# Kernel optimization log

Measured on AMD Instinct MI355X. Metric: run time of the kernel, lower is better.

The kernel has to match this reference:

```python
import jax, jax.numpy as jnp
import numpy as np

EPSILON = 0.001  # clip margin from HParams.epsilon
_EPS32 = float(np.finfo(np.float32).eps)  # added to bound in create_ops


@jax.custom_jvp
def floor_ste(x):
    """Floor with Straight-Through-Estimator gradient."""
    return jnp.floor(x)


@floor_ste.defjvp
def _floor_ste_jvp(primals, tangents):
    (x,), (t,) = primals, tangents
    return jnp.floor(x), t


def _binarize(x, bound):
    # (-inf,0) -> -bound/2, [0,inf) -> +bound/2, via scale-clip-floor-STE
    scale = 1.0 / bound
    clip_bound = 1.0 - EPSILON
    y = jnp.clip(x * scale, -clip_bound, clip_bound)
    y = floor_ste(y) + 0.5
    return (y / scale).astype(x.dtype)


def setup_inputs() -> dict:
    key = jax.random.key(0)
    k1, k2 = jax.random.split(key, 2)
    B, S, D, F = 4, 4096, 2048, 8192
    inputs = jax.random.normal(k1, (B, S, D), dtype=jnp.float32)
    # lecun_normal init: std = 1/sqrt(fan_in)
    kernel = jax.random.normal(k2, (D, F), dtype=jnp.float32) * (1.0 / np.sqrt(D))
    bias = jnp.zeros((F,), dtype=jnp.float32)
    return {"inputs": inputs, "kernel": kernel, "bias": bias}


def reference(inputs, kernel, bias):
    # weight bound: max |W| over contraction axes (axis 0), shape (1, F)
    w_bound = jax.lax.stop_gradient(
        jnp.max(jnp.abs(kernel), axis=0, keepdims=True) + _EPS32)
    k_bin = _binarize(kernel, w_bound)
    # input bound: max |x| over contraction axis (last), per-row, shape (B, S, 1)
    a_bound = jax.lax.stop_gradient(
        jnp.max(jnp.abs(inputs), axis=-1, keepdims=True) + _EPS32)
    x_bin = _binarize(inputs, a_bound)
    out = jnp.einsum('bsd,df->bsf', x_bin, k_bin)  # [B, S, F]
    return out + bias
```

## Files before the change

### kernel.cpp

```cpp
#include <hip/hip_runtime.h>
#include <stdint.h>

#define MDIM 16384
#define NDIM 8192
#define KDIM 2048
#define KB2 1024
#define EPS32 1.1920928955078125e-07f
#define BM 256
#define BN 256

using i32x4 = __attribute__((ext_vector_type(4))) int;
using i32x8 = __attribute__((ext_vector_type(8))) int;
using f32x4 = __attribute__((ext_vector_type(4))) float;
using f32x16 = __attribute__((ext_vector_type(16))) float;
typedef __attribute__((address_space(3))) const int8_t* lds_cptr;

__device__ __forceinline__ void gload_lds16(const void* g, void* l) {
  __builtin_amdgcn_global_load_lds(
      (const __attribute__((address_space(1))) void*)g,
      (__attribute__((address_space(3))) void*)l,
      16, 0, 0);
}

__device__ __forceinline__ uint32_t nib(float v) { return (v < 0.f) ? 0xAu : 0x2u; }

__global__ __launch_bounds__(256) void k_pack(const float* __restrict__ x,
                                              const float* __restrict__ W,
                                              uint8_t* __restrict__ As,
                                              uint8_t* __restrict__ Bs,
                                              float* __restrict__ ab,
                                              unsigned int* __restrict__ wbu) {
  __shared__ uint8_t sm[64 * 68];
  __shared__ float red[4][64];
  const int t = threadIdx.x;
  if (blockIdx.x < MDIM) {
    const int m = blockIdx.x;
    const float4* row = (const float4*)(x + (size_t)m * KDIM);
    const float4 v0 = row[2 * t];
    const float4 v1 = row[2 * t + 1];
    const uint32_t pk =
        nib(v0.x) | (nib(v0.y) << 4) | (nib(v0.z) << 8) | (nib(v0.w) << 12) |
        (nib(v1.x) << 16) | (nib(v1.y) << 20) | (nib(v1.z) << 24) | (nib(v1.w) << 28);
    ((uint32_t*)(As + (size_t)m * KB2))[t] = pk;
    float mx = fmaxf(fmaxf(fabsf(v0.x), fabsf(v0.y)), fmaxf(fabsf(v0.z), fabsf(v0.w)));
    mx = fmaxf(mx, fmaxf(fmaxf(fabsf(v1.x), fabsf(v1.y)), fmaxf(fabsf(v1.z), fabsf(v1.w))));
#pragma unroll
    for (int o = 32; o > 0; o >>= 1) mx = fmaxf(mx, __shfl_xor(mx, o, 64));
    if ((t & 63) == 0) red[0][t >> 6] = mx;
    __syncthreads();
    if (t == 0)
      ab[m] = fmaxf(fmaxf(red[0][0], red[0][1]), fmaxf(red[0][2], red[0][3])) + EPS32;
  } else {
    const int bid = blockIdx.x - MDIM;
    const int bd = bid & 31;
    const int bf = bid >> 5;
    const int d0 = bd * 64, f0 = bf * 64;
    const int fl = t & 63, dq = t >> 6;
    float mx = 0.f;
#pragma unroll
    for (int i = 0; i < 16; ++i) {
      const int dl = i * 4 + dq;
      const float v = W[(size_t)(d0 + dl) * NDIM + f0 + fl];
      sm[fl * 68 + dl] = (uint8_t)nib(v);
      mx = fmaxf(mx, fabsf(v));
    }
    red[dq][fl] = mx;
    __syncthreads();
    if (t < 64) {
      const float r = fmaxf(fmaxf(red[0][t], red[1][t]), fmaxf(red[2][t], red[3][t]));
      atomicMax(&wbu[f0 + t], __float_as_uint(r));
    }
    const int nl = t >> 2, ch = t & 3;
    const uint8_t* s = &sm[nl * 68 + ch * 16];
    uint32_t w0 = 0, w1 = 0;
#pragma unroll
    for (int i = 0; i < 4; ++i)
      w0 |= (uint32_t)(s[2 * i] | (s[2 * i + 1] << 4)) << (8 * i);
#pragma unroll
    for (int i = 0; i < 4; ++i)
      w1 |= (uint32_t)(s[8 + 2 * i] | (s[9 + 2 * i] << 4)) << (8 * i);
    *(uint2*)(Bs + (size_t)(f0 + nl) * KB2 + (d0 >> 1) + ch * 8) = make_uint2(w0, w1);
  }
}

__global__ __launch_bounds__(512, 2) void k_gemm(const uint8_t* __restrict__ As,
                                                 const uint8_t* __restrict__ Bs,
                                                 const float* __restrict__ ab,
                                                 const float* __restrict__ wbf,
                                                 const float* __restrict__ bias,
                                                 float* __restrict__ out) {
  __shared__ int8_t lds[4][32768];
  const int t = threadIdx.x;
  const int lane = t & 63, wid = t >> 6;
  const int bid = blockIdx.x;
  const int xcd = bid & 7;
  const int local = bid >> 3;
  const int bnin = local & 7;
  const int bml = (local >> 3) & 7;
  const int bnc = local >> 6;
  const int bm = xcd * 8 + bml;
  const int bn = bnc * 8 + bnin;
  const size_t m0 = (size_t)bm * BM, n0 = (size_t)bn * BN;
  const int wr = wid >> 2, wc = wid & 3;

  const int r4 = lane >> 2;
  const int sl0 = (lane & 3) ^ ((lane >> 5) & 1);
  const int sl1 = sl0 ^ 2;
  const uint8_t* gA0 = As + (m0 + (size_t)(wid * 32 + r4)) * KB2 + sl0 * 16;
  const uint8_t* gA1 = As + (m0 + (size_t)(wid * 32 + 16 + r4)) * KB2 + sl1 * 16;
  const uint8_t* gB0 = Bs + (n0 + (size_t)(wid * 32 + r4)) * KB2 + sl0 * 16;
  const uint8_t* gB1 = Bs + (n0 + (size_t)(wid * 32 + 16 + r4)) * KB2 + sl1 * 16;

  const int l31 = lane & 31, h = lane >> 5;
  const int xs = (l31 >> 3) & 3;
  const int aoff0 = (wr * 128 + l31) * 64 + ((h ^ xs) * 16);
  const int aoff1 = (wr * 128 + l31) * 64 + (((2 + h) ^ xs) * 16);
  const int boff0 = 16384 + (wc * 64 + l31) * 64 + ((h ^ xs) * 16);
  const int boff1 = 16384 + (wc * 64 + l31) * 64 + (((2 + h) ^ xs) * 16);

  f32x16 acc[4][2];
#pragma unroll
  for (int i = 0; i < 4; ++i)
#pragma unroll
    for (int j = 0; j < 2; ++j) acc[i][j] = (f32x16){0};

#define ISSUE_A(u)                                      \
  do {                                                  \
    int8_t* dA = &lds[(u) & 3][wid * 2048];             \
    gload_lds16(gA0 + (size_t)(u) * 64, dA);            \
    gload_lds16(gA1 + (size_t)(u) * 64, dA + 1024);     \
  } while (0)
#define ISSUE_B(u)                                      \
  do {                                                  \
    int8_t* dB = &lds[(u) & 3][16384 + wid * 2048];     \
    gload_lds16(gB0 + (size_t)(u) * 64, dB);            \
    gload_lds16(gB1 + (size_t)(u) * 64, dB + 1024);     \
  } while (0)

#define DSR(dst, ptr, OFF) \
  asm volatile("ds_read_b128 %0, %1 offset:" #OFF : "=v"(dst) : "v"(ptr))

#define FRAG(x) __builtin_shufflevector((x), (x), 0, 1, 2, 3, -1, -1, -1, -1)

#define SMFMA(D, BF, AF)                                                     \
  D = __builtin_amdgcn_mfma_scale_f32_32x32x64_f8f6f4(                       \
      FRAG(BF), FRAG(AF), D, 4, 4, 0, 0x7F7F7F7F, 0, 0x7F7F7F7F)

#define MP(I, B0, B1, AF) SMFMA(acc[I][0], B0, AF); SMFMA(acc[I][1], B1, AF)

#define LGK(N)                                              \
  asm volatile("s_waitcnt lgkmcnt(" #N ")" ::: "memory");   \
  __builtin_amdgcn_sched_barrier(0);

#define ITER(TT, DOISSUE, WAIT_TAIL)                                          \
  {                                                                           \
    const int8_t* sb = &lds[(TT) & 3][0];                                     \
    lds_cptr pA0 = (lds_cptr)(sb + aoff0);                                    \
    lds_cptr pA1 = (lds_cptr)(sb + aoff1);                                    \
    lds_cptr pB0 = (lds_cptr)(sb + boff0);                                    \
    lds_cptr pB1 = (lds_cptr)(sb + boff1);                                    \
    i32x4 a0, a1, a2, a3, a4, a5, a6, a7, b0, b1, b2, b3;                     \
    if (DOISSUE) { ISSUE_A((TT) + 3); ISSUE_B((TT) + 3); }                    \
    DSR(a0, pA0, 0); DSR(b0, pB0, 0); DSR(b1, pB0, 2048);                     \
    DSR(a1, pA0, 2048); DSR(a2, pA0, 4096); DSR(a3, pA0, 6144);               \
    DSR(a4, pA1, 0); DSR(b2, pB1, 0); DSR(b3, pB1, 2048);                     \
    DSR(a5, pA1, 2048); DSR(a6, pA1, 4096); DSR(a7, pA1, 6144);               \
    LGK(9); __builtin_amdgcn_s_setprio(1); MP(0, b0, b1, a0);                 \
    LGK(8); MP(1, b0, b1, a1);                                                \
    LGK(7); MP(2, b0, b1, a2);                                                \
    LGK(6); MP(3, b0, b1, a3);                                                \
    LGK(3); MP(0, b2, b3, a4);                                                \
    LGK(2); MP(1, b2, b3, a5);                                                \
    LGK(1); MP(2, b2, b3, a6);                                                \
    LGK(0); MP(3, b2, b3, a7);                                                \
    __builtin_amdgcn_s_setprio(0);                                            \
    asm volatile(WAIT_TAIL ::: "memory");                                     \
    __builtin_amdgcn_s_barrier();                                             \
  }

  ISSUE_A(0); ISSUE_B(0);
  ISSUE_A(1); ISSUE_B(1);
  ISSUE_A(2); ISSUE_B(2);
  asm volatile("s_waitcnt vmcnt(8)" ::: "memory");
  __builtin_amdgcn_s_barrier();

#pragma unroll 2
  for (int tt = 0; tt < 12; ++tt) ITER(tt, true, "s_waitcnt vmcnt(8)");
  ITER(12, true, "s_waitcnt vmcnt(8)");
  ITER(13, false, "s_waitcnt vmcnt(4)");
  ITER(14, false, "s_waitcnt vmcnt(0)");
  ITER(15, false, "s_nop 0");

#pragma unroll
  for (int i = 0; i < 4; ++i) {
    const size_t m = m0 + wr * 128 + i * 32 + l31;
    const float av = 0.25f * ab[m];
    float* orow = out + m * NDIM;
#pragma unroll
    for (int j = 0; j < 2; ++j) {
#pragma unroll
      for (int q = 0; q < 4; ++q) {
        const size_t nb = n0 + wc * 64 + j * 32 + q * 8 + h * 4;
        const f32x4 wv = *(const f32x4*)&wbf[nb];
        const f32x4 bv = *(const f32x4*)&bias[nb];
        f32x4 o;
        o[0] = av * ((wv[0] + EPS32) * acc[i][j][q * 4 + 0]) + bv[0];
        o[1] = av * ((wv[1] + EPS32) * acc[i][j][q * 4 + 1]) + bv[1];
        o[2] = av * ((wv[2] + EPS32) * acc[i][j][q * 4 + 2]) + bv[2];
        o[3] = av * ((wv[3] + EPS32) * acc[i][j][q * 4 + 3]) + bv[3];
        *(f32x4*)(orow + nb) = o;
      }
    }
  }
#undef ITER
#undef LGK
#undef MP
#undef SMFMA
#undef FRAG
#undef DSR
#undef ISSUE_A
#undef ISSUE_B
}

extern "C" void kernel_launch(void* const* d_in, const int* in_sizes, int n_in,
                              void* d_out, int out_size, void* d_ws, size_t ws_size,
                              hipStream_t stream) {
  const float* x = (const float*)d_in[0];
  const float* W = (const float*)d_in[1];
  const float* bias = (const float*)d_in[2];
  float* out = (float*)d_out;

  char* ws = (char*)d_ws;
  uint8_t* As = (uint8_t*)ws;
  uint8_t* Bs = (uint8_t*)(ws + (size_t)(16u << 20));
  float* ab = (float*)(ws + (size_t)(24u << 20));
  float* wb = (float*)(ws + (size_t)(24u << 20) + (1u << 16));

  (void)hipMemsetAsync(wb, 0, NDIM * sizeof(float), stream);
  k_pack<<<MDIM + (KDIM / 64) * (NDIM / 64), 256, 0, stream>>>(x, W, As, Bs, ab,
                                                               (unsigned int*)wb);
  k_gemm<<<(MDIM / BM) * (NDIM / BN), 512, 0, stream>>>(As, Bs, ab, wb, bias, out);
}
```

Baseline: 308.4 us.

## Double-buffer LDS fragments in registers to overlap reads with MFMAs

Restructures the GEMM main loop into a software pipeline. Each iteration now issues the LDS fragment reads for the next K-tile into an alternate register set, then runs the current tile's MFMAs from registers loaded in the previous iteration. The per-iteration lgkmcnt staircase and tail wait are replaced by a single head wait (lgkmcnt(0) plus vmcnt) and a barrier. The goal is to hide LDS read latency behind matrix math. The cost is roughly 96 extra VGPRs held live for the second fragment set, plus a prologue read.

```diff
diff --git a/kernel.cpp b/kernel.cpp
--- a/kernel.cpp
+++ b/kernel.cpp
@@ -10,7 +10,6 @@
 #define BN 256
 
 using i32x4 = __attribute__((ext_vector_type(4))) int;
-using i32x8 = __attribute__((ext_vector_type(8))) int;
 using f32x4 = __attribute__((ext_vector_type(4))) float;
 using f32x16 = __attribute__((ext_vector_type(16))) float;
 typedef __attribute__((address_space(3))) const int8_t* lds_cptr;
@@ -124,15 +123,15 @@
 #pragma unroll
     for (int j = 0; j < 2; ++j) acc[i][j] = (f32x16){0};
 
-#define ISSUE_A(u)                                      \
+  i32x4 ea0, ea1, ea2, ea3, ea4, ea5, ea6, ea7, eb0, eb1, eb2, eb3;
+  i32x4 oa0, oa1, oa2, oa3, oa4, oa5, oa6, oa7, ob0, ob1, ob2, ob3;
+
+#define ISSUE(u)                                        \
   do {                                                  \
     int8_t* dA = &lds[(u) & 3][wid * 2048];             \
+    int8_t* dB = &lds[(u) & 3][16384 + wid * 2048];     \
     gload_lds16(gA0 + (size_t)(u) * 64, dA);            \
     gload_lds16(gA1 + (size_t)(u) * 64, dA + 1024);     \
-  } while (0)
-#define ISSUE_B(u)                                      \
-  do {                                                  \
-    int8_t* dB = &lds[(u) & 3][16384 + wid * 2048];     \
     gload_lds16(gB0 + (size_t)(u) * 64, dB);            \
     gload_lds16(gB1 + (size_t)(u) * 64, dB + 1024);     \
   } while (0)
@@ -140,56 +139,77 @@
 #define DSR(dst, ptr, OFF) \
   asm volatile("ds_read_b128 %0, %1 offset:" #OFF : "=v"(dst) : "v"(ptr))
 
-#define FRAG(x) __builtin_shufflevector((x), (x), 0, 1, 2, 3, -1, -1, -1, -1)
-
-#define SMFMA(D, BF, AF)                                                     \
-  D = __builtin_amdgcn_mfma_scale_f32_32x32x64_f8f6f4(                       \
-      FRAG(BF), FRAG(AF), D, 4, 4, 0, 0x7F7F7F7F, 0, 0x7F7F7F7F)
-
-#define MP(I, B0, B1, AF) SMFMA(acc[I][0], B0, AF); SMFMA(acc[I][1], B1, AF)
-
-#define LGK(N)                                              \
-  asm volatile("s_waitcnt lgkmcnt(" #N ")" ::: "memory");   \
-  __builtin_amdgcn_sched_barrier(0);
-
-#define ITER(TT, DOISSUE, WAIT_TAIL)                                          \
+#define READS(SLOT, A0, A1, A2, A3, A4, A5, A6, A7, B0, B1, B2, B3)           \
   {                                                                           \
-    const int8_t* sb = &lds[(TT) & 3][0];                                     \
+    const int8_t* sb = &lds[(SLOT)][0];                                       \
     lds_cptr pA0 = (lds_cptr)(sb + aoff0);                                    \
     lds_cptr pA1 = (lds_cptr)(sb + aoff1);                                    \
     lds_cptr pB0 = (lds_cptr)(sb + boff0);                                    \
     lds_cptr pB1 = (lds_cptr)(sb + boff1);                                    \
-    i32x4 a0, a1, a2, a3, a4, a5, a6, a7, b0, b1, b2, b3;                     \
-    if (DOISSUE) { ISSUE_A((TT) + 3); ISSUE_B((TT) + 3); }                    \
-    DSR(a0, pA0, 0); DSR(b0, pB0, 0); DSR(b1, pB0, 2048);                     \
-    DSR(a1, pA0, 2048); DSR(a2, pA0, 4096); DSR(a3, pA0, 6144);               \
-    DSR(a4, pA1, 0); DSR(b2, pB1, 0); DSR(b3, pB1, 2048);                     \
-    DSR(a5, pA1, 2048); DSR(a6, pA1, 4096); DSR(a7, pA1, 6144);               \
-    LGK(9); __builtin_amdgcn_s_setprio(1); MP(0, b0, b1, a0);                 \
-    LGK(8); MP(1, b0, b1, a1);                                                \
-    LGK(7); MP(2, b0, b1, a2);                                                \
-    LGK(6); MP(3, b0, b1, a3);                                                \
-    LGK(3); MP(0, b2, b3, a4);                                                \
-    LGK(2); MP(1, b2, b3, a5);                                                \
-    LGK(1); MP(2, b2, b3, a6);                                                \
-    LGK(0); MP(3, b2, b3, a7);                                                \
+    DSR(A0, pA0, 0); DSR(B0, pB0, 0); DSR(B1, pB0, 2048);                     \
+    DSR(A1, pA0, 2048); DSR(A2, pA0, 4096); DSR(A3, pA0, 6144);               \
+    DSR(A4, pA1, 0); DSR(B2, pB1, 0); DSR(B3, pB1, 2048);                     \
+    DSR(A5, pA1, 2048); DSR(A6, pA1, 4096); DSR(A7, pA1, 6144);               \
+  }
+
+#define FRAG(x) __builtin_shufflevector((x), (x), 0, 1, 2, 3, -1, -1, -1, -1)
+
+#define SMFMA(D, BF, AF)                                                      \
+  D = __builtin_amdgcn_mfma_scale_f32_32x32x64_f8f6f4(                        \
+      FRAG(BF), FRAG(AF), D, 4, 4, 0, 0x7F7F7F7F, 0, 0x7F7F7F7F)
+
+#define MFMAS(A0, A1, A2, A3, A4, A5, A6, A7, B0, B1, B2, B3)                 \
+  SMFMA(acc[0][0], B0, A0); SMFMA(acc[0][1], B1, A0);                         \
+  SMFMA(acc[1][0], B0, A1); SMFMA(acc[1][1], B1, A1);                         \
+  SMFMA(acc[2][0], B0, A2); SMFMA(acc[2][1], B1, A2);                         \
+  SMFMA(acc[3][0], B0, A3); SMFMA(acc[3][1], B1, A3);                         \
+  SMFMA(acc[0][0], B2, A4); SMFMA(acc[0][1], B3, A4);                         \
+  SMFMA(acc[1][0], B2, A5); SMFMA(acc[1][1], B3, A5);                         \
+  SMFMA(acc[2][0], B2, A6); SMFMA(acc[2][1], B3, A6);                         \
+  SMFMA(acc[3][0], B2, A7); SMFMA(acc[3][1], B3, A7);
+
+#define HEAD(VM)                                                  \
+  asm volatile("s_waitcnt lgkmcnt(0)" ::: "memory");              \
+  asm volatile("s_waitcnt vmcnt(" #VM ")" ::: "memory");          \
+  __builtin_amdgcn_sched_barrier(0);                              \
+  __builtin_amdgcn_s_barrier();
+
+#define ITER_E(TT, DOISSUE, DOREAD, VM)                                       \
+  {                                                                           \
+    HEAD(VM);                                                                 \
+    if (DOISSUE) ISSUE((TT) + 3);                                             \
+    if (DOREAD)                                                               \
+      READS(((TT) + 1) & 3, oa0, oa1, oa2, oa3, oa4, oa5, oa6, oa7,           \
+            ob0, ob1, ob2, ob3);                                              \
+    __builtin_amdgcn_s_setprio(1);                                            \
+    MFMAS(ea0, ea1, ea2, ea3, ea4, ea5, ea6, ea7, eb0, eb1, eb2, eb3);        \
     __builtin_amdgcn_s_setprio(0);                                            \
-    asm volatile(WAIT_TAIL ::: "memory");                                     \
-    __builtin_amdgcn_s_barrier();                                             \
-  }
-
-  ISSUE_A(0); ISSUE_B(0);
-  ISSUE_A(1); ISSUE_B(1);
-  ISSUE_A(2); ISSUE_B(2);
+  }
+#define ITER_O(TT, DOISSUE, DOREAD, VM)                                       \
+  {                                                                           \
+    HEAD(VM);                                                                 \
+    if (DOISSUE) ISSUE((TT) + 3);                                             \
+    if (DOREAD)                                                               \
+      READS(((TT) + 1) & 3, ea0, ea1, ea2, ea3, ea4, ea5, ea6, ea7,           \
+            eb0, eb1, eb2, eb3);                                              \
+    __builtin_amdgcn_s_setprio(1);                                            \
+    MFMAS(oa0, oa1, oa2, oa3, oa4, oa5, oa6, oa7, ob0, ob1, ob2, ob3);        \
+    __builtin_amdgcn_s_setprio(0);                                            \
+  }
+
+  ISSUE(0); ISSUE(1); ISSUE(2);
   asm volatile("s_waitcnt vmcnt(8)" ::: "memory");
   __builtin_amdgcn_s_barrier();
-
-#pragma unroll 2
-  for (int tt = 0; tt < 12; ++tt) ITER(tt, true, "s_waitcnt vmcnt(8)");
-  ITER(12, true, "s_waitcnt vmcnt(8)");
-  ITER(13, false, "s_waitcnt vmcnt(4)");
-  ITER(14, false, "s_waitcnt vmcnt(0)");
-  ITER(15, false, "s_nop 0");
+  READS(0, ea0, ea1, ea2, ea3, ea4, ea5, ea6, ea7, eb0, eb1, eb2, eb3);
+
+  for (int tt = 0; tt < 12; tt += 2) {
+    ITER_E(tt, 1, 1, 4);
+    ITER_O(tt + 1, 1, 1, 4);
+  }
+  ITER_E(12, 1, 1, 4);
+  ITER_O(13, 0, 1, 4);
+  ITER_E(14, 0, 1, 0);
+  ITER_O(15, 0, 0, 0);
 
 #pragma unroll
   for (int i = 0; i < 4; ++i) {
@@ -212,14 +232,15 @@
       }
     }
   }
-#undef ITER
-#undef LGK
-#undef MP
+#undef ITER_E
+#undef ITER_O
+#undef HEAD
+#undef MFMAS
 #undef SMFMA
 #undef FRAG
+#undef READS
 #undef DSR
-#undef ISSUE_A
-#undef ISSUE_B
+#undef ISSUE
 }
 
 extern "C" void kernel_launch(void* const* d_in, const int* in_sizes, int n_in,
```

New measurement: 307.1 us. No clear change (-0.4%).

## Replace direct global-to-LDS loads with register-staged loads and ds_write pipeline

Applied to the files above, without the earlier changes.

Replaces the global_load_lds direct-to-LDS path with global_load_dwordx4 into registers, then explicit ds_write_b128 into a 4-slot LDS ring. Two register sets alternate between even and odd iterations. The swizzle moves from the global address side to the LDS write address. The aim is to avoid the limits of the direct LDS load path, such as 16-byte granularity and M0 setup, and to get finer control over the overlap between loads and MFMA. In exchange it uses more VGPRs, and the inline-asm waits may be fragile, for example when the compiler reorders or when lgkmcnt counts mix with ds_write traffic.

```diff
diff --git a/kernel.cpp b/kernel.cpp
--- a/kernel.cpp
+++ b/kernel.cpp
@@ -10,17 +10,10 @@
 #define BN 256
 
 using i32x4 = __attribute__((ext_vector_type(4))) int;
-using i32x8 = __attribute__((ext_vector_type(8))) int;
 using f32x4 = __attribute__((ext_vector_type(4))) float;
 using f32x16 = __attribute__((ext_vector_type(16))) float;
 typedef __attribute__((address_space(3))) const int8_t* lds_cptr;
-
-__device__ __forceinline__ void gload_lds16(const void* g, void* l) {
-  __builtin_amdgcn_global_load_lds(
-      (const __attribute__((address_space(1))) void*)g,
-      (__attribute__((address_space(3))) void*)l,
-      16, 0, 0);
-}
+typedef __attribute__((address_space(3))) int8_t* lds_ptr;
 
 __device__ __forceinline__ uint32_t nib(float v) { return (v < 0.f) ? 0xAu : 0x2u; }
 
@@ -104,12 +97,16 @@
   const int wr = wid >> 2, wc = wid & 3;
 
   const int r4 = lane >> 2;
-  const int sl0 = (lane & 3) ^ ((lane >> 5) & 1);
-  const int sl1 = sl0 ^ 2;
-  const uint8_t* gA0 = As + (m0 + (size_t)(wid * 32 + r4)) * KB2 + sl0 * 16;
-  const uint8_t* gA1 = As + (m0 + (size_t)(wid * 32 + 16 + r4)) * KB2 + sl1 * 16;
-  const uint8_t* gB0 = Bs + (n0 + (size_t)(wid * 32 + r4)) * KB2 + sl0 * 16;
-  const uint8_t* gB1 = Bs + (n0 + (size_t)(wid * 32 + 16 + r4)) * KB2 + sl1 * 16;
+  const int c4 = lane & 3;
+  const uint8_t* glA0 = As + (m0 + (size_t)(wid * 32 + r4)) * KB2 + c4 * 16;
+  const uint8_t* glA1 = As + (m0 + (size_t)(wid * 32 + 16 + r4)) * KB2 + c4 * 16;
+  const uint8_t* glB0 = Bs + (n0 + (size_t)(wid * 32 + r4)) * KB2 + c4 * 16;
+  const uint8_t* glB1 = Bs + (n0 + (size_t)(wid * 32 + 16 + r4)) * KB2 + c4 * 16;
+  const int xs0 = (lane >> 5) & 1;
+  const int wsl0 = (c4 ^ xs0) * 16;
+  const int wsl1 = (c4 ^ (xs0 ^ 2)) * 16;
+  const int wrowA0 = (wid * 32 + r4) * 64 + wsl0;
+  const int wrowA1 = (wid * 32 + 16 + r4) * 64 + wsl1;
 
   const int l31 = lane & 31, h = lane >> 5;
   const int xs = (l31 >> 3) & 3;
@@ -124,43 +121,59 @@
 #pragma unroll
     for (int j = 0; j < 2; ++j) acc[i][j] = (f32x16){0};
 
-#define ISSUE_A(u)                                      \
-  do {                                                  \
-    int8_t* dA = &lds[(u) & 3][wid * 2048];             \
-    gload_lds16(gA0 + (size_t)(u) * 64, dA);            \
-    gload_lds16(gA1 + (size_t)(u) * 64, dA + 1024);     \
+  i32x4 sE0, sE1, sE2, sE3, sO0, sO1, sO2, sO3;
+
+#define GLOAD(dst, p) \
+  asm volatile("global_load_dwordx4 %0, %1, off" : "=v"(dst) : "v"(p))
+
+#define GL4(u, S0, S1, S2, S3)                  \
+  do {                                          \
+    GLOAD(S0, glA0 + (size_t)(u) * 64);         \
+    GLOAD(S1, glA1 + (size_t)(u) * 64);         \
+    GLOAD(S2, glB0 + (size_t)(u) * 64);         \
+    GLOAD(S3, glB1 + (size_t)(u) * 64);         \
   } while (0)
-#define ISSUE_B(u)                                      \
-  do {                                                  \
-    int8_t* dB = &lds[(u) & 3][16384 + wid * 2048];     \
-    gload_lds16(gB0 + (size_t)(u) * 64, dB);            \
-    gload_lds16(gB1 + (size_t)(u) * 64, dB + 1024);     \
+
+#define DSW(addr, val, OFF) \
+  asm volatile("ds_write_b128 %0, %1 offset:" #OFF :: "v"(addr), "v"(val))
+
+#define WR4(u, S0, S1, S2, S3)                              \
+  do {                                                      \
+    lds_ptr w0 = (lds_ptr)&lds[(u) & 3][0] + wrowA0;        \
+    lds_ptr w1 = (lds_ptr)&lds[(u) & 3][0] + wrowA1;        \
+    DSW(w0, S0, 0);                                         \
+    DSW(w1, S1, 0);                                         \
+    DSW(w0, S2, 16384);                                     \
+    DSW(w1, S3, 16384);                                     \
   } while (0)
+
+#define VMW(N)                                              \
+  asm volatile("s_waitcnt vmcnt(" #N ")" ::: "memory");     \
+  __builtin_amdgcn_sched_barrier(0);
 
 #define DSR(dst, ptr, OFF) \
   asm volatile("ds_read_b128 %0, %1 offset:" #OFF : "=v"(dst) : "v"(ptr))
-
-#define FRAG(x) __builtin_shufflevector((x), (x), 0, 1, 2, 3, -1, -1, -1, -1)
-
-#define SMFMA(D, BF, AF)                                                     \
-  D = __builtin_amdgcn_mfma_scale_f32_32x32x64_f8f6f4(                       \
-      FRAG(BF), FRAG(AF), D, 4, 4, 0, 0x7F7F7F7F, 0, 0x7F7F7F7F)
-
-#define MP(I, B0, B1, AF) SMFMA(acc[I][0], B0, AF); SMFMA(acc[I][1], B1, AF)
 
 #define LGK(N)                                              \
   asm volatile("s_waitcnt lgkmcnt(" #N ")" ::: "memory");   \
   __builtin_amdgcn_sched_barrier(0);
 
-#define ITER(TT, DOISSUE, WAIT_TAIL)                                          \
+#define FRAG(x) __builtin_shufflevector((x), (x), 0, 1, 2, 3, -1, -1, -1, -1)
+
+#define SMFMA(D, BF, AF)                                                      \
+  D = __builtin_amdgcn_mfma_scale_f32_32x32x64_f8f6f4(                        \
+      FRAG(BF), FRAG(AF), D, 4, 4, 0, 0x7F7F7F7F, 0, 0x7F7F7F7F)
+
+#define MP(I, B0, B1, AF) SMFMA(acc[I][0], B0, AF); SMFMA(acc[I][1], B1, AF)
+
+#define LADDER(SLOT)                                                          \
   {                                                                           \
-    const int8_t* sb = &lds[(TT) & 3][0];                                     \
+    const int8_t* sb = &lds[(SLOT)][0];                                       \
     lds_cptr pA0 = (lds_cptr)(sb + aoff0);                                    \
     lds_cptr pA1 = (lds_cptr)(sb + aoff1);                                    \
     lds_cptr pB0 = (lds_cptr)(sb + boff0);                                    \
     lds_cptr pB1 = (lds_cptr)(sb + boff1);                                    \
     i32x4 a0, a1, a2, a3, a4, a5, a6, a7, b0, b1, b2, b3;                     \
-    if (DOISSUE) { ISSUE_A((TT) + 3); ISSUE_B((TT) + 3); }                    \
     DSR(a0, pA0, 0); DSR(b0, pB0, 0); DSR(b1, pB0, 2048);                     \
     DSR(a1, pA0, 2048); DSR(a2, pA0, 4096); DSR(a3, pA0, 6144);               \
     DSR(a4, pA1, 0); DSR(b2, pB1, 0); DSR(b3, pB1, 2048);                     \
@@ -174,22 +187,42 @@
     LGK(1); MP(2, b2, b3, a6);                                                \
     LGK(0); MP(3, b2, b3, a7);                                                \
     __builtin_amdgcn_s_setprio(0);                                            \
-    asm volatile(WAIT_TAIL ::: "memory");                                     \
+  }
+
+#define ITER_EVEN(TT, DOLOAD, VMN)                                            \
+  {                                                                           \
     __builtin_amdgcn_s_barrier();                                             \
-  }
-
-  ISSUE_A(0); ISSUE_B(0);
-  ISSUE_A(1); ISSUE_B(1);
-  ISSUE_A(2); ISSUE_B(2);
-  asm volatile("s_waitcnt vmcnt(8)" ::: "memory");
-  __builtin_amdgcn_s_barrier();
-
-#pragma unroll 2
-  for (int tt = 0; tt < 12; ++tt) ITER(tt, true, "s_waitcnt vmcnt(8)");
-  ITER(12, true, "s_waitcnt vmcnt(8)");
-  ITER(13, false, "s_waitcnt vmcnt(4)");
-  ITER(14, false, "s_waitcnt vmcnt(0)");
-  ITER(15, false, "s_nop 0");
+    if (DOLOAD) GL4((TT) + 3, sO0, sO1, sO2, sO3);                            \
+    VMW(VMN);                                                                 \
+    WR4((TT) + 2, sE0, sE1, sE2, sE3);                                        \
+    LADDER((TT) & 3);                                                         \
+  }
+#define ITER_ODD(TT, DOLOAD, VMN)                                             \
+  {                                                                           \
+    __builtin_amdgcn_s_barrier();                                             \
+    if (DOLOAD) GL4((TT) + 3, sE0, sE1, sE2, sE3);                            \
+    VMW(VMN);                                                                 \
+    WR4((TT) + 2, sO0, sO1, sO2, sO3);                                        \
+    LADDER((TT) & 3);                                                         \
+  }
+
+  GL4(0, sE0, sE1, sE2, sE3);
+  VMW(0);
+  WR4(0, sE0, sE1, sE2, sE3);
+  GL4(1, sO0, sO1, sO2, sO3);
+  VMW(0);
+  WR4(1, sO0, sO1, sO2, sO3);
+  asm volatile("s_waitcnt lgkmcnt(0)" ::: "memory");
+  GL4(2, sE0, sE1, sE2, sE3);
+
+  for (int tt = 0; tt < 12; tt += 2) {
+    ITER_EVEN(tt, 1, 4);
+    ITER_ODD(tt + 1, 1, 4);
+  }
+  ITER_EVEN(12, 1, 4);
+  ITER_ODD(13, 0, 0);
+  { __builtin_amdgcn_s_barrier(); LADDER(2); }
+  { __builtin_amdgcn_s_barrier(); LADDER(3); }
 
 #pragma unroll
   for (int i = 0; i < 4; ++i) {
@@ -212,14 +245,19 @@
       }
     }
   }
-#undef ITER
-#undef LGK
+#undef ITER_EVEN
+#undef ITER_ODD
+#undef LADDER
 #undef MP
 #undef SMFMA
 #undef FRAG
+#undef LGK
 #undef DSR
-#undef ISSUE_A
-#undef ISSUE_B
+#undef VMW
+#undef WR4
+#undef DSW
+#undef GL4
+#undef GLOAD
 }
 
 extern "C" void kernel_launch(void* const* d_in, const int* in_sizes, int n_in,
```

New measurement: 303.9 us, median of 2. Within noise of the previous version (-1.5%).

## Shrink GEMM tiles to 128x128 with simple double-buffered loop

Applied to the files above, without the earlier changes.

The FP4 scaled-MFMA GEMM moves from 256x256 tiles with 512 threads and a 4-stage LDS pipeline to 128x128 tiles with 256 threads and 2-stage double buffering. It aims for higher occupancy and a smaller per-block LDS footprint. The hand-scheduled ds_read/lgkmcnt interleaving and priority hints are replaced by plain C++ loads and __syncthreads. The cost is twice the global/L2 operand traffic per output, a shallower prefetch, and compiler-chosen instruction scheduling.

```diff
diff --git a/kernel.cpp b/kernel.cpp
--- a/kernel.cpp
+++ b/kernel.cpp
@@ -6,14 +6,13 @@
 #define KDIM 2048
 #define KB2 1024
 #define EPS32 1.1920928955078125e-07f
-#define BM 256
-#define BN 256
+#define BM 128
+#define BN 128
 
 using i32x4 = __attribute__((ext_vector_type(4))) int;
 using i32x8 = __attribute__((ext_vector_type(8))) int;
 using f32x4 = __attribute__((ext_vector_type(4))) float;
 using f32x16 = __attribute__((ext_vector_type(16))) float;
-typedef __attribute__((address_space(3))) const int8_t* lds_cptr;
 
 __device__ __forceinline__ void gload_lds16(const void* g, void* l) {
   __builtin_amdgcn_global_load_lds(
@@ -83,25 +82,25 @@
   }
 }
 
-__global__ __launch_bounds__(512, 2) void k_gemm(const uint8_t* __restrict__ As,
+__global__ __launch_bounds__(256, 4) void k_gemm(const uint8_t* __restrict__ As,
                                                  const uint8_t* __restrict__ Bs,
                                                  const float* __restrict__ ab,
                                                  const float* __restrict__ wbf,
                                                  const float* __restrict__ bias,
                                                  float* __restrict__ out) {
-  __shared__ int8_t lds[4][32768];
+  __shared__ int8_t lds[2][16384];
   const int t = threadIdx.x;
   const int lane = t & 63, wid = t >> 6;
   const int bid = blockIdx.x;
   const int xcd = bid & 7;
   const int local = bid >> 3;
   const int bnin = local & 7;
-  const int bml = (local >> 3) & 7;
-  const int bnc = local >> 6;
-  const int bm = xcd * 8 + bml;
+  const int bml = (local >> 3) & 15;
+  const int bnc = local >> 7;
+  const int bm = xcd * 16 + bml;
   const int bn = bnc * 8 + bnin;
   const size_t m0 = (size_t)bm * BM, n0 = (size_t)bn * BN;
-  const int wr = wid >> 2, wc = wid & 3;
+  const int wr = wid >> 1, wc = wid & 1;
 
   const int r4 = lane >> 2;
   const int sl0 = (lane & 3) ^ ((lane >> 5) & 1);
@@ -113,87 +112,61 @@
 
   const int l31 = lane & 31, h = lane >> 5;
   const int xs = (l31 >> 3) & 3;
-  const int aoff0 = (wr * 128 + l31) * 64 + ((h ^ xs) * 16);
-  const int aoff1 = (wr * 128 + l31) * 64 + (((2 + h) ^ xs) * 16);
-  const int boff0 = 16384 + (wc * 64 + l31) * 64 + ((h ^ xs) * 16);
-  const int boff1 = 16384 + (wc * 64 + l31) * 64 + (((2 + h) ^ xs) * 16);
-
-  f32x16 acc[4][2];
-#pragma unroll
-  for (int i = 0; i < 4; ++i)
+  const int aoff0 = (wr * 64 + l31) * 64 + ((h ^ xs) * 16);
+  const int aoff1 = (wr * 64 + l31) * 64 + (((2 + h) ^ xs) * 16);
+  const int boff0 = 8192 + (wc * 64 + l31) * 64 + ((h ^ xs) * 16);
+  const int boff1 = 8192 + (wc * 64 + l31) * 64 + (((2 + h) ^ xs) * 16);
+
+  f32x16 acc[2][2];
+#pragma unroll
+  for (int i = 0; i < 2; ++i)
 #pragma unroll
     for (int j = 0; j < 2; ++j) acc[i][j] = (f32x16){0};
 
-#define ISSUE_A(u)                                      \
+#define ISSUE(u)                                        \
   do {                                                  \
-    int8_t* dA = &lds[(u) & 3][wid * 2048];             \
+    int8_t* dA = &lds[(u) & 1][wid * 2048];             \
+    int8_t* dB = &lds[(u) & 1][8192 + wid * 2048];      \
     gload_lds16(gA0 + (size_t)(u) * 64, dA);            \
     gload_lds16(gA1 + (size_t)(u) * 64, dA + 1024);     \
-  } while (0)
-#define ISSUE_B(u)                                      \
-  do {                                                  \
-    int8_t* dB = &lds[(u) & 3][16384 + wid * 2048];     \
     gload_lds16(gB0 + (size_t)(u) * 64, dB);            \
     gload_lds16(gB1 + (size_t)(u) * 64, dB + 1024);     \
   } while (0)
 
-#define DSR(dst, ptr, OFF) \
-  asm volatile("ds_read_b128 %0, %1 offset:" #OFF : "=v"(dst) : "v"(ptr))
-
-#define FRAG(x) __builtin_shufflevector((x), (x), 0, 1, 2, 3, -1, -1, -1, -1)
-
-#define SMFMA(D, BF, AF)                                                     \
-  D = __builtin_amdgcn_mfma_scale_f32_32x32x64_f8f6f4(                       \
-      FRAG(BF), FRAG(AF), D, 4, 4, 0, 0x7F7F7F7F, 0, 0x7F7F7F7F)
-
-#define MP(I, B0, B1, AF) SMFMA(acc[I][0], B0, AF); SMFMA(acc[I][1], B1, AF)
-
-#define LGK(N)                                              \
-  asm volatile("s_waitcnt lgkmcnt(" #N ")" ::: "memory");   \
-  __builtin_amdgcn_sched_barrier(0);
-
-#define ITER(TT, DOISSUE, WAIT_TAIL)                                          \
-  {                                                                           \
-    const int8_t* sb = &lds[(TT) & 3][0];                                     \
-    lds_cptr pA0 = (lds_cptr)(sb + aoff0);                                    \
-    lds_cptr pA1 = (lds_cptr)(sb + aoff1);                                    \
-    lds_cptr pB0 = (lds_cptr)(sb + boff0);                                    \
-    lds_cptr pB1 = (lds_cptr)(sb + boff1);                                    \
-    i32x4 a0, a1, a2, a3, a4, a5, a6, a7, b0, b1, b2, b3;                     \
-    if (DOISSUE) { ISSUE_A((TT) + 3); ISSUE_B((TT) + 3); }                    \
-    DSR(a0, pA0, 0); DSR(b0, pB0, 0); DSR(b1, pB0, 2048);                     \
-    DSR(a1, pA0, 2048); DSR(a2, pA0, 4096); DSR(a3, pA0, 6144);               \
-    DSR(a4, pA1, 0); DSR(b2, pB1, 0); DSR(b3, pB1, 2048);                     \
-    DSR(a5, pA1, 2048); DSR(a6, pA1, 4096); DSR(a7, pA1, 6144);               \
-    LGK(9); __builtin_amdgcn_s_setprio(1); MP(0, b0, b1, a0);                 \
-    LGK(8); MP(1, b0, b1, a1);                                                \
-    LGK(7); MP(2, b0, b1, a2);                                                \
-    LGK(6); MP(3, b0, b1, a3);                                                \
-    LGK(3); MP(0, b2, b3, a4);                                                \
-    LGK(2); MP(1, b2, b3, a5);                                                \
-    LGK(1); MP(2, b2, b3, a6);                                                \
-    LGK(0); MP(3, b2, b3, a7);                                                \
-    __builtin_amdgcn_s_setprio(0);                                            \
-    asm volatile(WAIT_TAIL ::: "memory");                                     \
-    __builtin_amdgcn_s_barrier();                                             \
+#define FR(x) __builtin_shufflevector((x), (x), 0, 1, 2, 3, -1, -1, -1, -1)
+
+#define SMFMA(D, BF, AF)                                                      \
+  D = __builtin_amdgcn_mfma_scale_f32_32x32x64_f8f6f4(                        \
+      FR(BF), FR(AF), D, 4, 4, 0, 0x7F7F7F7F, 0, 0x7F7F7F7F)
+
+  ISSUE(0);
+  __syncthreads();
+
+  for (int tt = 0; tt < 16; ++tt) {
+    if (tt < 15) ISSUE(tt + 1);
+    const int8_t* sb = &lds[tt & 1][0];
+    i32x4 a0 = *(const i32x4*)(sb + aoff0);
+    i32x4 a1 = *(const i32x4*)(sb + aoff0 + 2048);
+    i32x4 b0 = *(const i32x4*)(sb + boff0);
+    i32x4 b1 = *(const i32x4*)(sb + boff0 + 2048);
+    SMFMA(acc[0][0], b0, a0);
+    SMFMA(acc[0][1], b1, a0);
+    SMFMA(acc[1][0], b0, a1);
+    SMFMA(acc[1][1], b1, a1);
+    i32x4 a2 = *(const i32x4*)(sb + aoff1);
+    i32x4 a3 = *(const i32x4*)(sb + aoff1 + 2048);
+    i32x4 b2 = *(const i32x4*)(sb + boff1);
+    i32x4 b3 = *(const i32x4*)(sb + boff1 + 2048);
+    SMFMA(acc[0][0], b2, a2);
+    SMFMA(acc[0][1], b3, a2);
+    SMFMA(acc[1][0], b2, a3);
+    SMFMA(acc[1][1], b3, a3);
+    __syncthreads();
   }
 
-  ISSUE_A(0); ISSUE_B(0);
-  ISSUE_A(1); ISSUE_B(1);
-  ISSUE_A(2); ISSUE_B(2);
-  asm volatile("s_waitcnt vmcnt(8)" ::: "memory");
-  __builtin_amdgcn_s_barrier();
-
-#pragma unroll 2
-  for (int tt = 0; tt < 12; ++tt) ITER(tt, true, "s_waitcnt vmcnt(8)");
-  ITER(12, true, "s_waitcnt vmcnt(8)");
-  ITER(13, false, "s_waitcnt vmcnt(4)");
-  ITER(14, false, "s_waitcnt vmcnt(0)");
-  ITER(15, false, "s_nop 0");
-
-#pragma unroll
-  for (int i = 0; i < 4; ++i) {
-    const size_t m = m0 + wr * 128 + i * 32 + l31;
+#pragma unroll
+  for (int i = 0; i < 2; ++i) {
+    const size_t m = m0 + wr * 64 + i * 32 + l31;
     const float av = 0.25f * ab[m];
     float* orow = out + m * NDIM;
 #pragma unroll
@@ -212,14 +185,9 @@
       }
     }
   }
-#undef ITER
-#undef LGK
-#undef MP
 #undef SMFMA
-#undef FRAG
-#undef DSR
-#undef ISSUE_A
-#undef ISSUE_B
+#undef FR
+#undef ISSUE
 }
 
 extern "C" void kernel_launch(void* const* d_in, const int* in_sizes, int n_in,
@@ -239,5 +207,5 @@
   (void)hipMemsetAsync(wb, 0, NDIM * sizeof(float), stream);
   k_pack<<<MDIM + (KDIM / 64) * (NDIM / 64), 256, 0, stream>>>(x, W, As, Bs, ab,
                                                                (unsigned int*)wb);
-  k_gemm<<<(MDIM / BM) * (NDIM / BN), 512, 0, stream>>>(As, Bs, ab, wb, bias, out);
-}
+  k_gemm<<<(MDIM / BM) * (NDIM / BN), 256, 0, stream>>>(As, Bs, ab, wb, bias, out);
+}
```

New measurement: 323.3 us. 1.05x slower.
